# Optimization experiments

Measured on AMD Instinct MI355X. Metric: run time of the kernel, lower is better.

## Reference

```python
import jax, jax.numpy as jnp
import numpy as np

N_NODES = 50000


def gcn_conv(x, src, dst, W, b):
    # PyG GCNConv: h = x @ W; out[i] = sum_j norm_ij * h[j] + b, with
    # symmetric normalization over the graph with self-loops (added by caller).
    deg = jax.ops.segment_sum(jnp.ones_like(dst, dtype=x.dtype), dst,
                              num_segments=N_NODES)
    dinv = jnp.where(deg > 0, jax.lax.rsqrt(deg), 0.0)
    norm = dinv[src] * dinv[dst]            # [E+N]
    h = x @ W                                # [N, out]
    msg = h[src] * norm[:, None]             # [E+N, out] gathered messages
    out = jax.ops.segment_sum(msg, dst, num_segments=N_NODES)
    return out + b


def setup_inputs() -> dict:
    key = jax.random.key(0)
    k1, k2, k3, k4, k5 = jax.random.split(key, 5)
    nfeat, nmid, nhid = 128, 128, 128
    x = jax.random.normal(k1, (N_NODES, nfeat), dtype=jnp.float32)
    edge_index = jax.random.randint(k2, (2, 800000), 0, N_NODES, dtype=jnp.int64)
    W1 = jax.random.normal(k3, (nfeat, nmid), dtype=jnp.float32) * 0.05
    b1 = jnp.zeros((nmid,), dtype=jnp.float32)
    W2 = jax.random.normal(k4, (nmid, nhid), dtype=jnp.float32) * 0.05
    b2 = jnp.zeros((nhid,), dtype=jnp.float32)
    return {"x": x, "edge_index": edge_index, "W1": W1, "b1": b1,
            "W2": W2, "b2": b2}


def reference(x, edge_index, W1, b1, W2, b2):
    # add self-loops once; both GCNConv layers use the same graph
    loops = jnp.arange(N_NODES, dtype=edge_index.dtype)
    src = jnp.concatenate([edge_index[0], loops])
    dst = jnp.concatenate([edge_index[1], loops])
    h = jax.nn.relu(gcn_conv(x, src, dst, W1, b1))
    h = jax.nn.relu(gcn_conv(h, src, dst, W2, b2))
    return h
```

## Files before the change

### kernel.cpp

```cpp
#include <hip/hip_runtime.h>
#include <hip/hip_fp16.h>

#define N_NODES 50000
#define F 128
#define RANGE 6250
#define LDK 136
#define PAD 64
#define GEMMB 391
#define CNTB 2048

typedef _Float16 f16x8 __attribute__((ext_vector_type(8)));
typedef float    f32x4 __attribute__((ext_vector_type(4)));

__global__ void k_prep(int* __restrict__ cnt,
                       const float* __restrict__ W1, const float* __restrict__ W2,
                       __half* __restrict__ Wt1, __half* __restrict__ Wt2) {
    const int b = blockIdx.x;
    if (b < 196) {
        const int i = b * 256 + threadIdx.x;
        if (i < N_NODES) cnt[i] = 0;
    } else {
        const float* W  = (b == 196) ? W1 : W2;
        __half*      Wt = (b == 196) ? Wt1 : Wt2;
        for (int i = threadIdx.x; i < F * F; i += 256) {
            const int k = i >> 7, n = i & 127;
            Wt[n * F + k] = __float2half(W[i]);
        }
    }
}

__device__ inline void gemm_tile(const float* __restrict__ X,
                                 const __half* __restrict__ Wt,
                                 const float* __restrict__ dinv,
                                 __half* __restrict__ Hs, int nrows, int r0,
                                 __half* Xs, __half* Ws) {
    const int t    = threadIdx.x;
    const int wid  = t >> 6;
    const int lane = t & 63;

    {
        const uint4* Wg = (const uint4*)Wt;
        const int n = t >> 2, c0 = (t & 3) * 4;
        uint4* drow = (uint4*)&Ws[n * LDK];
#pragma unroll
        for (int j = 0; j < 4; ++j) drow[c0 + j] = Wg[n * 16 + c0 + j];
    }
    {
        const int xr = t >> 2, c0 = (t & 3) * 32;
        const int grow = min(r0 + xr, nrows - 1);
        const float4* Xg = (const float4*)(X + (size_t)grow * F);
        __half2* xd = (__half2*)&Xs[xr * LDK + c0];
#pragma unroll
        for (int j = 0; j < 8; ++j) {
            const float4 v = Xg[c0 / 4 + j];
            xd[2 * j]     = __float22half2_rn(make_float2(v.x, v.y));
            xd[2 * j + 1] = __float22half2_rn(make_float2(v.z, v.w));
        }
    }
    __syncthreads();

    const int m  = lane & 15;
    const int kg = lane >> 4;
    f32x4 acc[8] = {};
#pragma unroll
    for (int kk = 0; kk < 4; ++kk) {
        const f16x8 a = *(const f16x8*)&Xs[(wid * 16 + m) * LDK + kk * 32 + kg * 8];
#pragma unroll
        for (int nt = 0; nt < 8; ++nt) {
            const f16x8 bfr = *(const f16x8*)&Ws[(nt * 16 + m) * LDK + kk * 32 + kg * 8];
            acc[nt] = __builtin_amdgcn_mfma_f32_16x16x32_f16(a, bfr, acc[nt], 0, 0, 0);
        }
    }
    __syncthreads();

    {
        const int lr0 = wid * 16 + kg * 4;
#pragma unroll
        for (int r = 0; r < 4; ++r) {
            const int lr = lr0 + r;
            const float dn = dinv ? dinv[min(r0 + lr, nrows - 1)] : 1.0f;
#pragma unroll
            for (int nt = 0; nt < 8; ++nt)
                Xs[lr * LDK + nt * 16 + m] = __float2half(dn * acc[nt][r]);
        }
    }
    __syncthreads();
    {
        const int row = t >> 2, c0 = (t & 3) * 4;
        const int g = r0 + row;
        if (g < nrows) {
            const uint4* srow = (const uint4*)&Xs[row * LDK];
            uint4* drow = (uint4*)(Hs + (size_t)g * F);
#pragma unroll
            for (int j = 0; j < 4; ++j) drow[c0 + j] = srow[c0 + j];
        }
    }
}

__global__ __launch_bounds__(512) void k_cg1(const float* __restrict__ X,
                                             const __half* __restrict__ Wt1,
                                             __half* __restrict__ Hs,
                                             const int* __restrict__ src,
                                             const int* __restrict__ dst, int E,
                                             int* __restrict__ cnt,
                                             unsigned short* __restrict__ csrP) {
    __shared__ __half Xs[128 * LDK];
    __shared__ __half Ws[128 * LDK];
    if (blockIdx.x < GEMMB) {
        gemm_tile(X, Wt1, nullptr, Hs, N_NODES, blockIdx.x * 128, Xs, Ws);
    } else {
        const int bid = blockIdx.x - GEMMB;
        const int r  = bid & 7;
        const int lo = r * RANGE, hi = min(lo + RANGE, N_NODES);
        const int base   = (bid >> 3) * 512 + threadIdx.x;
        const int stride = (CNTB >> 3) * 512;
        for (int i = base; i < E; i += stride) {
            const int d = dst[i];
            const int s = src[i];
            if (d >= lo && d < hi) {
                const int pos = atomicAdd(&cnt[d], 1);
                if (pos < PAD) csrP[d * PAD + pos] = (unsigned short)s;
            }
        }
    }
}

__global__ __launch_bounds__(512) void k_sdv(const int* __restrict__ cnt,
                                             float* __restrict__ dinv,
                                             __half* __restrict__ Hs) {
    const int tid = blockIdx.x * 512 + threadIdx.x;
    const int nth = gridDim.x * 512;
    for (int n = tid; n < N_NODES; n += nth)
        dinv[n] = rsqrtf((float)(cnt[n] + 1));
    uint4* __restrict__ Hv = (uint4*)Hs;
    const int total = N_NODES * 16;
    for (int i = tid; i < total; i += nth) {
        const float dn = rsqrtf((float)(cnt[i >> 4] + 1));
        uint4 v = Hv[i];
        __half2* h = (__half2*)&v;
#pragma unroll
        for (int j = 0; j < 4; ++j) {
            float2 f = __half22float2(h[j]);
            h[j] = __float22half2_rn(make_float2(dn * f.x, dn * f.y));
        }
        Hv[i] = v;
    }
}

__global__ __launch_bounds__(512) void k_gemm(const float* __restrict__ X,
                                              const __half* __restrict__ Wt,
                                              const float* __restrict__ dinv,
                                              __half* __restrict__ Hs, int nrows) {
    __shared__ __half Xs[128 * LDK];
    __shared__ __half Ws[128 * LDK];
    gemm_tile(X, Wt, dinv, Hs, nrows, blockIdx.x * 128, Xs, Ws);
}

__global__ __launch_bounds__(256) void k_gather(const int* __restrict__ cnt,
                                                const unsigned short* __restrict__ csrP,
                                                const __half* __restrict__ Hs,
                                                const float* __restrict__ dinv,
                                                const float* __restrict__ b,
                                                float* __restrict__ out) {
    const int tid = blockIdx.x * blockDim.x + threadIdx.x;
    const int g   = tid >> 5;
    const int l32 = threadIdx.x & 31;
    const int ng  = (gridDim.x * blockDim.x) >> 5;
    const uint2* __restrict__ Hv = (const uint2*)Hs;
    float4* __restrict__ outv = (float4*)out;
    const float4 bb = ((const float4*)b)[l32];
    for (int n = g; n < N_NODES; n += ng) {
        const int beg = n * PAD;
        const int end = beg + min(cnt[n], PAD);
        float4 a0 = make_float4(0.f, 0.f, 0.f, 0.f);
        float4 a1 = make_float4(0.f, 0.f, 0.f, 0.f);
        float4 a2 = make_float4(0.f, 0.f, 0.f, 0.f);
        float4 a3 = make_float4(0.f, 0.f, 0.f, 0.f);
        {
            const uint2 raw = Hv[n * 32 + l32];
            const float2 f0 = __half22float2(*(const __half2*)&raw.x);
            const float2 f1 = __half22float2(*(const __half2*)&raw.y);
            a0.x += f0.x; a0.y += f0.y; a0.z += f1.x; a0.w += f1.y;
        }
        int e = beg;
        for (; e + 3 < end; e += 4) {
            const int s0 = csrP[e];
            const int s1 = csrP[e + 1];
            const int s2 = csrP[e + 2];
            const int s3 = csrP[e + 3];
            const uint2 r0 = Hv[s0 * 32 + l32];
            const uint2 r1 = Hv[s1 * 32 + l32];
            const uint2 r2 = Hv[s2 * 32 + l32];
            const uint2 r3 = Hv[s3 * 32 + l32];
            float2 f;
            f = __half22float2(*(const __half2*)&r0.x); a0.x += f.x; a0.y += f.y;
            f = __half22float2(*(const __half2*)&r0.y); a0.z += f.x; a0.w += f.y;
            f = __half22float2(*(const __half2*)&r1.x); a1.x += f.x; a1.y += f.y;
            f = __half22float2(*(const __half2*)&r1.y); a1.z += f.x; a1.w += f.y;
            f = __half22float2(*(const __half2*)&r2.x); a2.x += f.x; a2.y += f.y;
            f = __half22float2(*(const __half2*)&r2.y); a2.z += f.x; a2.w += f.y;
            f = __half22float2(*(const __half2*)&r3.x); a3.x += f.x; a3.y += f.y;
            f = __half22float2(*(const __half2*)&r3.y); a3.z += f.x; a3.w += f.y;
        }
        for (; e < end; ++e) {
            const uint2 r0 = Hv[csrP[e] * 32 + l32];
            float2 f;
            f = __half22float2(*(const __half2*)&r0.x); a1.x += f.x; a1.y += f.y;
            f = __half22float2(*(const __half2*)&r0.y); a1.z += f.x; a1.w += f.y;
        }
        const float dn = dinv[n];
        float4 o;
        o.x = fmaxf(fmaf(dn, (a0.x + a1.x) + (a2.x + a3.x), bb.x), 0.f);
        o.y = fmaxf(fmaf(dn, (a0.y + a1.y) + (a2.y + a3.y), bb.y), 0.f);
        o.z = fmaxf(fmaf(dn, (a0.z + a1.z) + (a2.z + a3.z), bb.z), 0.f);
        o.w = fmaxf(fmaf(dn, (a0.w + a1.w) + (a2.w + a3.w), bb.w), 0.f);
        outv[n * 32 + l32] = o;
    }
}

extern "C" void kernel_launch(void* const* d_in, const int* in_sizes, int n_in,
                              void* d_out, int out_size, void* d_ws, size_t ws_size,
                              hipStream_t stream) {
    const float* x  = (const float*)d_in[0];
    const int*   ei = (const int*)  d_in[1];
    const float* W1 = (const float*)d_in[2];
    const float* b1 = (const float*)d_in[3];
    const float* W2 = (const float*)d_in[4];
    const float* b2 = (const float*)d_in[5];
    float* out = (float*)d_out;

    const int E = in_sizes[1] / 2;
    const int* srcp = ei;
    const int* dstp = ei + E;

    int*            cnt  = (int*)d_ws;
    float*          dinv = (float*)(cnt + N_NODES);
    unsigned short* csrP = (unsigned short*)(dinv + N_NODES);
    __half*         Hs   = (__half*)(csrP + (size_t)N_NODES * PAD);
    __half*         Wt1  = Hs + (size_t)N_NODES * F;
    __half*         Wt2  = Wt1 + F * F;

    k_prep  <<<198, 256, 0, stream>>>(cnt, W1, W2, Wt1, Wt2);
    k_cg1   <<<GEMMB + CNTB, 512, 0, stream>>>(x, Wt1, Hs, srcp, dstp, E, cnt, csrP);
    k_sdv   <<<256, 512, 0, stream>>>(cnt, dinv, Hs);
    k_gather<<<2048, 256, 0, stream>>>(cnt, csrP, Hs, dinv, b1, out);
    k_gemm  <<<GEMMB, 512, 0, stream>>>(out, Wt2, dinv, Hs, N_NODES);
    k_gather<<<2048, 256, 0, stream>>>(cnt, csrP, Hs, dinv, b2, out);
}
```

Measured before the change: 157.9 us.

## Use XCC-aware dynamic work queues for edge bucketing in counting phase

Replaces the static assignment of counting blocks to destination ranges with per-range atomic chunk queues. Each block reads its XCC id so that it starts on the range matching its chiplet, which keeps the atomics for one range mostly inside one L2, and it then steals chunks from the other ranges. This targets load imbalance and cross-XCC atomic traffic on the cnt and csrP arrays. In exchange it adds a global atomic and two block barriers per 1024-edge chunk, and blocks from other XCCs still touch every range once their own queue is empty.

```diff
diff --git a/kernel.cpp b/kernel.cpp
--- a/kernel.cpp
+++ b/kernel.cpp
@@ -8,17 +8,19 @@
 #define PAD 64
 #define GEMMB 391
 #define CNTB 2048
+#define CH 1024
 
 typedef _Float16 f16x8 __attribute__((ext_vector_type(8)));
 typedef float    f32x4 __attribute__((ext_vector_type(4)));
 
-__global__ void k_prep(int* __restrict__ cnt,
+__global__ void k_prep(int* __restrict__ cnt, int* __restrict__ q,
                        const float* __restrict__ W1, const float* __restrict__ W2,
                        __half* __restrict__ Wt1, __half* __restrict__ Wt2) {
     const int b = blockIdx.x;
     if (b < 196) {
         const int i = b * 256 + threadIdx.x;
         if (i < N_NODES) cnt[i] = 0;
+        if (b == 0 && threadIdx.x < 8) q[threadIdx.x] = 0;
     } else {
         const float* W  = (b == 196) ? W1 : W2;
         __half*      Wt = (b == 196) ? Wt1 : Wt2;
@@ -103,23 +105,35 @@
                                              const int* __restrict__ src,
                                              const int* __restrict__ dst, int E,
                                              int* __restrict__ cnt,
-                                             unsigned short* __restrict__ csrP) {
+                                             unsigned short* __restrict__ csrP,
+                                             int* __restrict__ q) {
     __shared__ __half Xs[128 * LDK];
     __shared__ __half Ws[128 * LDK];
     if (blockIdx.x < GEMMB) {
         gemm_tile(X, Wt1, nullptr, Hs, N_NODES, blockIdx.x * 128, Xs, Ws);
     } else {
-        const int bid = blockIdx.x - GEMMB;
-        const int r  = bid & 7;
-        const int lo = r * RANGE, hi = min(lo + RANGE, N_NODES);
-        const int base   = (bid >> 3) * 512 + threadIdx.x;
-        const int stride = (CNTB >> 3) * 512;
-        for (int i = base; i < E; i += stride) {
-            const int d = dst[i];
-            const int s = src[i];
-            if (d >= lo && d < hi) {
-                const int pos = atomicAdd(&cnt[d], 1);
-                if (pos < PAD) csrP[d * PAD + pos] = (unsigned short)s;
+        int xcc;
+        asm volatile("s_getreg_b32 %0, hwreg(HW_REG_XCC_ID)" : "=s"(xcc));
+        __shared__ int s_chunk;
+        const int nchunk = (E + CH - 1) / CH;
+        for (int a = 0; a < 8; ++a) {
+            const int r  = (xcc + a) & 7;
+            const int lo = r * RANGE, hi = min(lo + RANGE, N_NODES);
+            for (;;) {
+                if (threadIdx.x == 0) s_chunk = atomicAdd(&q[r], 1);
+                __syncthreads();
+                const int c = s_chunk;
+                __syncthreads();
+                if (c >= nchunk) break;
+                const int e1 = min(c * CH + CH, E);
+                for (int i = c * CH + threadIdx.x; i < e1; i += 512) {
+                    const int d = dst[i];
+                    const int s = src[i];
+                    if (d >= lo && d < hi) {
+                        const int pos = atomicAdd(&cnt[d], 1);
+                        if (pos < PAD) csrP[d * PAD + pos] = (unsigned short)s;
+                    }
+                }
             }
         }
     }
@@ -235,13 +249,14 @@
 
     int*            cnt  = (int*)d_ws;
     float*          dinv = (float*)(cnt + N_NODES);
-    unsigned short* csrP = (unsigned short*)(dinv + N_NODES);
+    int*            q    = (int*)(dinv + N_NODES);
+    unsigned short* csrP = (unsigned short*)(q + 16);
     __half*         Hs   = (__half*)(csrP + (size_t)N_NODES * PAD);
     __half*         Wt1  = Hs + (size_t)N_NODES * F;
     __half*         Wt2  = Wt1 + F * F;
 
-    k_prep  <<<198, 256, 0, stream>>>(cnt, W1, W2, Wt1, Wt2);
-    k_cg1   <<<GEMMB + CNTB, 512, 0, stream>>>(x, Wt1, Hs, srcp, dstp, E, cnt, csrP);
+    k_prep  <<<198, 256, 0, stream>>>(cnt, q, W1, W2, Wt1, Wt2);
+    k_cg1   <<<GEMMB + CNTB, 512, 0, stream>>>(x, Wt1, Hs, srcp, dstp, E, cnt, csrP, q);
     k_sdv   <<<256, 512, 0, stream>>>(cnt, dinv, Hs);
     k_gather<<<2048, 256, 0, stream>>>(cnt, csrP, Hs, dinv, b1, out);
     k_gemm  <<<GEMMB, 512, 0, stream>>>(out, Wt2, dinv, Hs, N_NODES);
```

Result: slower. 395.9 us (+150.6%).
